# Kernel optimization log

Hardware: AMD Instinct MI355X
Metric: run time of the kernel (lower is better)

Reference implementation:

```python
import jax, jax.numpy as jnp
import numpy as np

N = 100000   # nodes
E = 1600000  # edges
NF = 128     # nfeat
NH = 64      # nhid
NC = 16      # nclass
C = 1.0      # curvature
EPS = 1e-15
PROJ_EPS = 4e-3  # float32 boundary eps used by HGCN PoincareBall
SQC = C ** 0.5


def _norm(v):
    return jnp.maximum(jnp.linalg.norm(v, axis=-1, keepdims=True), EPS)


def _artanh(v):
    return jnp.arctanh(jnp.clip(v, -1.0 + 1e-7, 1.0 - 1e-7))


def proj(p):
    # clip to the open ball of radius (1-eps)/sqrt(c)
    n = _norm(p)
    maxnorm = (1.0 - PROJ_EPS) / SQC
    return jnp.where(n > maxnorm, p / n * maxnorm, p)


def expmap0(u):
    n = _norm(u)
    return jnp.tanh(SQC * n) * u / (SQC * n)


def logmap0(p):
    n = _norm(p)
    return _artanh(SQC * n) * p / (SQC * n)


def mobius_add(x, y):
    x2 = jnp.sum(x * x, axis=-1, keepdims=True)
    y2 = jnp.sum(y * y, axis=-1, keepdims=True)
    xy = jnp.sum(x * y, axis=-1, keepdims=True)
    num = (1.0 + 2.0 * C * xy + C * y2) * x + (1.0 - C * x2) * y
    den = 1.0 + 2.0 * C * xy + (C ** 2) * x2 * y2
    return num / jnp.maximum(den, EPS)


def mobius_matvec(W, p):
    # W: [out, in], p: [N, in] on the ball
    pn = _norm(p)
    mp = p @ W.T  # [N, out]
    mpn = jnp.linalg.norm(mp, axis=-1, keepdims=True)
    res = jnp.tanh(mpn / pn * _artanh(SQC * pn)) * mp / (SQC * jnp.maximum(mpn, EPS))
    return jnp.where(mpn <= EPS, jnp.zeros_like(res), res)


def setup_inputs() -> dict:
    key = jax.random.key(0)
    ks = jax.random.split(key, 16)
    inp = {
        "x": jax.random.normal(ks[0], (N, NF), dtype=jnp.float32),
        "src": jax.random.randint(ks[1], (E,), 0, N, dtype=jnp.int32),
        "dst": jax.random.randint(ks[2], (E,), 0, N, dtype=jnp.int32),
        "adj_val": jax.random.uniform(ks[3], (E,), dtype=jnp.float32) * 0.0625,
        "W1": jax.random.normal(ks[4], (NH, NF), dtype=jnp.float32) / np.sqrt(NF),
        "b1": jnp.zeros((NH,), dtype=jnp.float32),
        "W2": jax.random.normal(ks[5], (NH, NH), dtype=jnp.float32) / np.sqrt(NH),
        "b2": jnp.zeros((NH,), dtype=jnp.float32),
        "W3": jax.random.normal(ks[6], (NH, NH), dtype=jnp.float32) / np.sqrt(NH),
        "b3": jnp.zeros((NH,), dtype=jnp.float32),
        "W4": jax.random.normal(ks[7], (NH // 2, NH), dtype=jnp.float32) / np.sqrt(NH),
        "b4": jnp.zeros((NH // 2,), dtype=jnp.float32),
        "W5": jax.random.normal(ks[8], (NC, NH // 2), dtype=jnp.float32) / np.sqrt(NH // 2),
        "b5": jnp.zeros((NC,), dtype=jnp.float32),
    }
    return inp


def _hgc_layer(h, W, b, src, dst, adj_val):
    # HypLinear: mobius matvec + hyperbolic bias
    res = proj(mobius_matvec(W, h))
    hyp_b = proj(expmap0(b[None, :]))
    res = proj(mobius_add(res, hyp_b))
    # HypAgg: aggregate in tangent space at origin via sparse adj
    ht = logmap0(res)                                   # [N, d]
    msg = adj_val[:, None] * ht[src]                    # [E, d]
    agg = jax.ops.segment_sum(msg, dst, num_segments=N)  # [N, d]
    res = proj(expmap0(agg))
    # HypAct: relu in tangent space, re-map to ball
    res = proj(expmap0(jax.nn.relu(logmap0(res))))
    return res


def reference(x, src, dst, adj_val, W1, b1, W2, b2, W3, b3, W4, b4, W5, b5):
    h = proj(expmap0(x))  # map Euclidean features to the ball (proj_tan0 = identity)
    h = _hgc_layer(h, W1, b1, src, dst, adj_val)
    h = _hgc_layer(h, W2, b2, src, dst, adj_val)
    h = _hgc_layer(h, W3, b3, src, dst, adj_val)
    t = logmap0(h)  # back to tangent space for the Euclidean head
    z = jax.nn.relu(t @ W4.T + b4)
    return jax.nn.log_softmax(z @ W5.T + b5, axis=-1)  # [N, nclass]
```

## Files before the change

### kernel.cpp

```cpp
#include <hip/hip_runtime.h>
#include <hip/hip_bf16.h>
#include <hip/hip_fp16.h>
#include <math.h>

#define NFEAT 128
#define NHID  64
#define ATH996 3.106303f
#define CHUNK 4096

typedef __attribute__((ext_vector_type(8))) short short8;
typedef __attribute__((ext_vector_type(4))) float floatx4;
typedef unsigned short ushort_t;
typedef unsigned long long u64;

__device__ __forceinline__ float wave_sum(float v) {
#pragma unroll
    for (int m = 1; m < 64; m <<= 1) v += __shfl_xor(v, m, 64);
    return v;
}

__device__ __forceinline__ float fast_tanh(float x) {
    float e = __expf(2.f * x);
    return 1.f - 2.f / (e + 1.f);
}

__device__ __forceinline__ float artanh_clip(float v) {
    const float lim = 0.99999988f;
    v = fminf(fmaxf(v, -lim), lim);
    return 0.5f * __logf((1.f + v) / (1.f - v));
}

__device__ __forceinline__ unsigned pack2(float a, float b) {
    __hip_bfloat16 x = __float2bfloat16(a), y = __float2bfloat16(b);
    ushort_t ux = *(ushort_t*)&x, uy = *(ushort_t*)&y;
    return (unsigned)ux | ((unsigned)uy << 16);
}

__device__ __forceinline__ ushort_t f2bf(float f) {
    __hip_bfloat16 h = __float2bfloat16(f);
    return *(ushort_t*)&h;
}

__device__ __forceinline__ float pe_adj(unsigned p) {
    return __half2float(__ushort_as_half((ushort_t)(p & 0x7fffu)));
}


__global__ __launch_bounds__(256) void k_bhist(const int* __restrict__ dst,
        int* __restrict__ gBktCnt, int e, int nb) {
    __shared__ int cnt[512];
    int tid = threadIdx.x;
    for (int t = tid; t < nb; t += 256) cnt[t] = 0;
    __syncthreads();
    int start = blockIdx.x * CHUNK, end = min(e, start + CHUNK);
    for (int i = start + tid; i < end; i += 256)
        atomicAdd(&cnt[dst[i] >> 8], 1);
    __syncthreads();
    for (int t = tid; t < nb; t += 256)
        if (cnt[t]) atomicAdd(&gBktCnt[t], cnt[t]);
}

__global__ __launch_bounds__(256) void k_bscan(const int* __restrict__ gBktCnt,
        int* __restrict__ gBktBase, int* __restrict__ gCur,
        int* __restrict__ off, int nb, int n, int e) {
    __shared__ int s[256];
    int tid = threadIdx.x;
    int base = tid * 4;
    int c0 = (base + 0 < nb) ? gBktCnt[base + 0] : 0;
    int c1 = (base + 1 < nb) ? gBktCnt[base + 1] : 0;
    int c2 = (base + 2 < nb) ? gBktCnt[base + 2] : 0;
    int c3 = (base + 3 < nb) ? gBktCnt[base + 3] : 0;
    int tsum = c0 + c1 + c2 + c3;
    s[tid] = tsum; __syncthreads();
    for (int o = 1; o < 256; o <<= 1) {
        int v = (tid >= o) ? s[tid - o] : 0;
        __syncthreads();
        s[tid] += v;
        __syncthreads();
    }
    int ex = s[tid] - tsum;
    int e0 = ex, e1 = ex + c0, e2 = ex + c0 + c1, e3 = ex + c0 + c1 + c2;
    if (base + 0 < nb) { gBktBase[base + 0] = e0; gCur[base + 0] = e0; }
    if (base + 1 < nb) { gBktBase[base + 1] = e1; gCur[base + 1] = e1; }
    if (base + 2 < nb) { gBktBase[base + 2] = e2; gCur[base + 2] = e2; }
    if (base + 3 < nb) { gBktBase[base + 3] = e3; gCur[base + 3] = e3; }
    if (tid == 255) gBktBase[nb] = s[255];
    if (tid == 0) off[n] = e;
}

__global__ __launch_bounds__(256) void k_bscatter(const int* __restrict__ dst,
        const int* __restrict__ src, const float* __restrict__ adj,
        int* __restrict__ gCur, u64* __restrict__ gStage, int e, int nb) {
    __shared__ u64 stage[CHUNK];
    __shared__ int cnt[512], excl[512], rcnt[512], myBase[512], s[256];
    int tid = threadIdx.x;
    int start = blockIdx.x * CHUNK, end = min(e, start + CHUNK);
    for (int t = tid; t < nb; t += 256) { cnt[t] = 0; rcnt[t] = 0; }
    __syncthreads();
    for (int i = start + tid; i < end; i += 256)
        atomicAdd(&cnt[dst[i] >> 8], 1);
    __syncthreads();
    int v0 = (2 * tid < nb) ? cnt[2 * tid] : 0;
    int v1 = (2 * tid + 1 < nb) ? cnt[2 * tid + 1] : 0;
    int tsum = v0 + v1;
    s[tid] = tsum; __syncthreads();
    for (int o = 1; o < 256; o <<= 1) {
        int v = (tid >= o) ? s[tid - o] : 0;
        __syncthreads();
        s[tid] += v;
        __syncthreads();
    }
    int ex = s[tid] - tsum;
    if (2 * tid < nb) excl[2 * tid] = ex;
    if (2 * tid + 1 < nb) excl[2 * tid + 1] = ex + v0;
    __syncthreads();
    for (int t = tid; t < nb; t += 256)
        if (cnt[t]) myBase[t] = atomicAdd(&gCur[t], cnt[t]);
    for (int i = start + tid; i < end; i += 256) {
        int d = dst[i];
        int b = d >> 8;
        unsigned ab = (unsigned)__half_as_ushort(__float2half(adj[i])) & 0x7fffu;
        u64 u = ((u64)(unsigned)d << 32) |
                (u64)(((unsigned)src[i] << 15) | ab);
        int r = atomicAdd(&rcnt[b], 1);
        stage[excl[b] + r] = u;
    }
    __syncthreads();
    int sz = end - start;
    for (int j = tid; j < sz; j += 256) {
        u64 u = stage[j];
        int b = (int)(u >> 40) & 0x1ff;
        gStage[myBase[b] + (j - excl[b])] = u;
    }
}

__global__ __launch_bounds__(256) void k_bfinal(const u64* __restrict__ gStage,
        const int* __restrict__ gBktBase, int* __restrict__ off,
        unsigned* __restrict__ pe, int n) {
    __shared__ int ncnt[256], nexcl[256], rcnt[256], s[256];
    int tid = threadIdx.x, b = blockIdx.x;
    int ebeg = gBktBase[b], eend = gBktBase[b + 1];
    int nbeg = b << 8;
    ncnt[tid] = 0; rcnt[tid] = 0;
    __syncthreads();
    for (int j = ebeg + tid; j < eend; j += 256) {
        int dl = ((int)(gStage[j] >> 32) & 0x1ffff) - nbeg;
        atomicAdd(&ncnt[dl], 1);
    }
    __syncthreads();
    int v = ncnt[tid];
    s[tid] = v; __syncthreads();
    for (int o = 1; o < 256; o <<= 1) {
        int t2 = (tid >= o) ? s[tid - o] : 0;
        __syncthreads();
        s[tid] += t2;
        __syncthreads();
    }
    nexcl[tid] = s[tid] - v;
    if (nbeg + tid < n) off[nbeg + tid] = ebeg + nexcl[tid];
    __syncthreads();
    for (int j = ebeg + tid; j < eend; j += 256) {
        u64 u = gStage[j];
        int dl = ((int)(u >> 32) & 0x1ffff) - nbeg;
        int r = atomicAdd(&rcnt[dl], 1);
        pe[ebeg + nexcl[dl] + r] = (unsigned)u;
    }
}

__global__ __launch_bounds__(256) void k_prep(
        const float* __restrict__ W1, const float* __restrict__ W2,
        const float* __restrict__ W3, const float* __restrict__ W4,
        const float* __restrict__ W5, const float* __restrict__ b1,
        const float* __restrict__ b2, const float* __restrict__ b3,
        ushort_t* __restrict__ Bpk1, ushort_t* __restrict__ Bpk2,
        ushort_t* __restrict__ Bpk3, ushort_t* __restrict__ Bpk4,
        ushort_t* __restrict__ Bpk5, float* __restrict__ hbs,
        float* __restrict__ hbns, int* __restrict__ gBktCnt, int nb) {
    int bid = blockIdx.x, tid = threadIdx.x;
    if (bid >= 75) {
        for (int t = tid; t < nb; t += 256) gBktCnt[t] = 0;
        return;
    }
    if (bid < 64) {
        const float* W; ushort_t* Bpk; int K, o;
        if (bid < 32)      { W = W1; Bpk = Bpk1; K = 128; o = bid * 256 + tid; }
        else if (bid < 48) { W = W2; Bpk = Bpk2; K = 64;  o = (bid - 32) * 256 + tid; }
        else               { W = W3; Bpk = Bpk3; K = 64;  o = (bid - 48) * 256 + tid; }
        int j = o & 7, c = (o >> 3) & 15, nf = (o >> 7) & 3, hi = (o >> 9) & 3,
            ks = o >> 11;
        Bpk[o] = f2bf(W[(nf * 16 + c) * K + ks * 32 + hi * 8 + j]);
    } else if (bid < 72) {
        int o = (bid - 64) * 256 + tid;
        int j = o & 7, c = (o >> 3) & 15, nf = (o >> 7) & 1, hi = (o >> 8) & 3,
            ks = o >> 10;
        Bpk4[o] = f2bf(W4[(nf * 16 + c) * 64 + ks * 32 + hi * 8 + j]);
    } else if (bid < 74) {
        int o = (bid - 72) * 256 + tid;
        if (o < 512) {
            int j = o & 7, c = (o >> 3) & 15, hi = o >> 7;
            Bpk5[o] = f2bf(W5[c * 32 + hi * 8 + j]);
        }
    } else {
        if (tid < 192) {
            int wv = tid >> 6, lane = tid & 63;
            const float* b = (wv == 0) ? b1 : (wv == 1) ? b2 : b3;
            float bv = b[lane];
            float bn = fmaxf(sqrtf(wave_sum(bv * bv)), 1e-15f);
            float th = fast_tanh(bn);
            float f = th / bn;
            float hn = th;
            if (th > 0.996f) { f = 0.996f / bn; hn = 0.996f; }
            hbs[wv * 64 + lane] = bv * f;
            if (lane == 0) hbns[wv] = hn;
        }
    }
}

__device__ __forceinline__ void epi_row(const floatx4* acc, int r, float pn,
        float hbn, const float* __restrict__ hb, int c, float outv[4]) {
    float pp = 0.f;
#pragma unroll
    for (int nf = 0; nf < 4; ++nf) pp += acc[nf][r] * acc[nf][r];
#pragma unroll
    for (int m = 1; m < 16; m <<= 1) pp += __shfl_xor(pp, m, 64);
    float mpn = sqrtf(pp);
    float an = artanh_clip(pn);
    if (hbn <= 1e-15f) {
        float targ = (mpn / pn) * an;
        float scale = (targ > ATH996) ? (ATH996 / mpn) : (an / pn);
        if (mpn <= 1e-15f) scale = 0.f;
#pragma unroll
        for (int nf = 0; nf < 4; ++nf) outv[nf] = acc[nf][r] * scale;
    } else {
        float targ = (mpn / pn) * an;
        float th = fast_tanh(targ);
        float rn = fminf(th, 0.996f);
        float rs = (mpn <= 1e-15f) ? 0.f : (rn / mpn);
        float res[4], xyp = 0.f;
#pragma unroll
        for (int nf = 0; nf < 4; ++nf) {
            res[nf] = acc[nf][r] * rs;
            xyp += res[nf] * hb[nf * 16 + c];
        }
#pragma unroll
        for (int m = 1; m < 16; m <<= 1) xyp += __shfl_xor(xyp, m, 64);
        float x2 = rn * rn, y2 = hbn * hbn;
        float den = fmaxf(1.f + 2.f * xyp + x2 * y2, 1e-15f);
        float ca = (1.f + 2.f * xyp + y2) / den, cb = (1.f - x2) / den;
        float mv[4], mm = 0.f;
#pragma unroll
        for (int nf = 0; nf < 4; ++nf) {
            mv[nf] = ca * res[nf] + cb * hb[nf * 16 + c];
            mm += mv[nf] * mv[nf];
        }
#pragma unroll
        for (int m = 1; m < 16; m <<= 1) mm += __shfl_xor(mm, m, 64);
        float mn = sqrtf(mm);
        float mc = fminf(fmaxf(mn, 1e-15f), 0.996f);
        float msc = ((mn > 0.996f) ? (0.996f / mn) : 1.f) * artanh_clip(mc) / mc;
#pragma unroll
        for (int nf = 0; nf < 4; ++nf) outv[nf] = mv[nf] * msc;
    }
}

__global__ __launch_bounds__(256) void k_gemm1(
        const float* __restrict__ x, const ushort_t* __restrict__ Bpk,
        const float* __restrict__ hb, const float* __restrict__ hbn_p,
        ushort_t* __restrict__ htout, int n) {
    constexpr int RB = 256;
    __shared__ __align__(16) unsigned char As[64 * RB];
    __shared__ float pns[64];
    int tid = threadIdx.x, wv = tid >> 6, lane = tid & 63;
    int rowBase = blockIdx.x * 64;
#pragma unroll
    for (int it = 0; it < 16; ++it) {
        int row = wv * 16 + it, rg = rowBase + row;
        float2 v = make_float2(0.f, 0.f);
        if (rg < n) v = *(const float2*)(x + (size_t)rg * NFEAT + lane * 2);
        float ss = wave_sum(v.x * v.x + v.y * v.y);
        float nr = fmaxf(sqrtf(ss), 1e-15f);
        float th = fast_tanh(nr);
        float f = th / nr;
        float pn = fmaxf(th, 1e-15f);
        if (th > 0.996f) { f = 0.996f / nr; pn = 0.996f; }
        unsigned byte = (unsigned)(row * RB + lane * 4) ^ ((row & 7) << 4);
        *(unsigned*)(As + byte) = pack2(v.x * f, v.y * f);
        if (lane == 0) pns[row] = pn;
    }
    int hi = lane >> 4, c = lane & 15;
    short8 bf[4][4];
#pragma unroll
    for (int ks = 0; ks < 4; ++ks)
#pragma unroll
        for (int nf = 0; nf < 4; ++nf)
            bf[ks][nf] = *(const short8*)(Bpk + (((size_t)(ks * 4 + hi) * 4 + nf) * 16 + c) * 8);
    floatx4 acc[4];
#pragma unroll
    for (int nf = 0; nf < 4; ++nf)
#pragma unroll
        for (int r = 0; r < 4; ++r) acc[nf][r] = 0.f;
    int arow = wv * 16 + c;
#pragma unroll
    for (int ks = 0; ks < 4; ++ks) {
        unsigned byte = (unsigned)(arow * RB + ks * 64 + hi * 16) ^ ((arow & 7) << 4);
        short8 af = *(const short8*)(As + byte);
#pragma unroll
        for (int nf = 0; nf < 4; ++nf)
            acc[nf] = __builtin_amdgcn_mfma_f32_16x16x32_bf16(af, bf[ks][nf], acc[nf], 0, 0, 0);
    }
    float hbn = hbn_p[0];
#pragma unroll
    for (int r = 0; r < 4; ++r) {
        int row = wv * 16 + hi * 4 + r, rg = rowBase + row;
        float outv[4];
        epi_row(acc, r, pns[row], hbn, hb, c, outv);
        if (rg < n) {
#pragma unroll
            for (int nf = 0; nf < 4; ++nf)
                htout[(size_t)rg * 64 + nf * 16 + c] = f2bf(outv[nf]);
        }
    }
}

__global__ __launch_bounds__(256) void k_gemm64(
        const ushort_t* __restrict__ h, const float* __restrict__ nrm_in,
        const ushort_t* __restrict__ Bpk, const float* __restrict__ hb,
        const float* __restrict__ hbn_p, ushort_t* __restrict__ htout, int n) {
    constexpr int RB = 128;
    __shared__ __align__(16) unsigned char As[64 * RB];
    int tid = threadIdx.x, wv = tid >> 6, lane = tid & 63;
    int rowBase = blockIdx.x * 64;
#pragma unroll
    for (int it = 0; it < 8; ++it) {
        int row = wv * 16 + it * 2 + (lane >> 5), rg = rowBase + row;
        int cl = lane & 31;
        unsigned pk = 0;
        if (rg < n) pk = *(const unsigned*)(h + (size_t)rg * 64 + cl * 2);
        unsigned byte = (unsigned)(row * RB + cl * 4) ^ ((row & 7) << 4);
        *(unsigned*)(As + byte) = pk;
    }
    int hi = lane >> 4, c = lane & 15;
    short8 bf[2][4];
#pragma unroll
    for (int ks = 0; ks < 2; ++ks)
#pragma unroll
        for (int nf = 0; nf < 4; ++nf)
            bf[ks][nf] = *(const short8*)(Bpk + (((size_t)(ks * 4 + hi) * 4 + nf) * 16 + c) * 8);
    floatx4 acc[4];
#pragma unroll
    for (int nf = 0; nf < 4; ++nf)
#pragma unroll
        for (int r = 0; r < 4; ++r) acc[nf][r] = 0.f;
    int arow = wv * 16 + c;
#pragma unroll
    for (int ks = 0; ks < 2; ++ks) {
        unsigned byte = (unsigned)(arow * RB + ks * 64 + hi * 16) ^ ((arow & 7) << 4);
        short8 af = *(const short8*)(As + byte);
#pragma unroll
        for (int nf = 0; nf < 4; ++nf)
            acc[nf] = __builtin_amdgcn_mfma_f32_16x16x32_bf16(af, bf[ks][nf], acc[nf], 0, 0, 0);
    }
    float hbn = hbn_p[0];
#pragma unroll
    for (int r = 0; r < 4; ++r) {
        int row = wv * 16 + hi * 4 + r, rg = rowBase + row;
        float pn = (rg < n) ? nrm_in[rg] : 1e-15f;
        float outv[4];
        epi_row(acc, r, pn, hbn, hb, c, outv);
        if (rg < n) {
#pragma unroll
            for (int nf = 0; nf < 4; ++nf)
                htout[(size_t)rg * 64 + nf * 16 + c] = f2bf(outv[nf]);
        }
    }
}

template <bool TANGENT_OUT>
__global__ __launch_bounds__(256) void k_agg_act(
        const ushort_t* __restrict__ ht, const int* __restrict__ off,
        const unsigned* __restrict__ pe, ushort_t* __restrict__ hout,
        float* __restrict__ nrm_out, int n) {
    int tid = threadIdx.x;
    int grp = tid >> 4, l = tid & 15;
    int node = blockIdx.x * 16 + grp;
    if (node >= n) return;
    int beg = off[node], end = off[node + 1];
    const char* hb8 = (const char*)ht + l * 8;
    float a0[4] = {0.f, 0.f, 0.f, 0.f};
    float a1[4] = {0.f, 0.f, 0.f, 0.f};
    float a2[4] = {0.f, 0.f, 0.f, 0.f};
    float a3[4] = {0.f, 0.f, 0.f, 0.f};
    int e = beg;
    for (; e + 3 < end; e += 4) {
        unsigned p0 = pe[e], p1 = pe[e + 1], p2 = pe[e + 2], p3 = pe[e + 3];
        uint2 r0 = *(const uint2*)(hb8 + ((size_t)(p0 >> 15) << 7));
        uint2 r1 = *(const uint2*)(hb8 + ((size_t)(p1 >> 15) << 7));
        uint2 r2 = *(const uint2*)(hb8 + ((size_t)(p2 >> 15) << 7));
        uint2 r3 = *(const uint2*)(hb8 + ((size_t)(p3 >> 15) << 7));
        float w0 = pe_adj(p0), w1 = pe_adj(p1), w2 = pe_adj(p2), w3 = pe_adj(p3);
        a0[0] = fmaf(w0, __uint_as_float(r0.x << 16), a0[0]);
        a0[1] = fmaf(w0, __uint_as_float(r0.x & 0xffff0000u), a0[1]);
        a0[2] = fmaf(w0, __uint_as_float(r0.y << 16), a0[2]);
        a0[3] = fmaf(w0, __uint_as_float(r0.y & 0xffff0000u), a0[3]);
        a1[0] = fmaf(w1, __uint_as_float(r1.x << 16), a1[0]);
        a1[1] = fmaf(w1, __uint_as_float(r1.x & 0xffff0000u), a1[1]);
        a1[2] = fmaf(w1, __uint_as_float(r1.y << 16), a1[2]);
        a1[3] = fmaf(w1, __uint_as_float(r1.y & 0xffff0000u), a1[3]);
        a2[0] = fmaf(w2, __uint_as_float(r2.x << 16), a2[0]);
        a2[1] = fmaf(w2, __uint_as_float(r2.x & 0xffff0000u), a2[1]);
        a2[2] = fmaf(w2, __uint_as_float(r2.y << 16), a2[2]);
        a2[3] = fmaf(w2, __uint_as_float(r2.y & 0xffff0000u), a2[3]);
        a3[0] = fmaf(w3, __uint_as_float(r3.x << 16), a3[0]);
        a3[1] = fmaf(w3, __uint_as_float(r3.x & 0xffff0000u), a3[1]);
        a3[2] = fmaf(w3, __uint_as_float(r3.y << 16), a3[2]);
        a3[3] = fmaf(w3, __uint_as_float(r3.y & 0xffff0000u), a3[3]);
    }
    for (; e < end; ++e) {
        unsigned p = pe[e];
        uint2 r = *(const uint2*)(hb8 + ((size_t)(p >> 15) << 7));
        float w = pe_adj(p);
        a0[0] = fmaf(w, __uint_as_float(r.x << 16), a0[0]);
        a0[1] = fmaf(w, __uint_as_float(r.x & 0xffff0000u), a0[1]);
        a0[2] = fmaf(w, __uint_as_float(r.y << 16), a0[2]);
        a0[3] = fmaf(w, __uint_as_float(r.y & 0xffff0000u), a0[3]);
    }
    float f0 = (a0[0] + a1[0]) + (a2[0] + a3[0]);
    float f1 = (a0[1] + a1[1]) + (a2[1] + a3[1]);
    float f2 = (a0[2] + a1[2]) + (a2[2] + a3[2]);
    float f3 = (a0[3] + a1[3]) + (a2[3] + a3[3]);
    float ss = f0 * f0 + f1 * f1 + f2 * f2 + f3 * f3;
#pragma unroll
    for (int m = 1; m < 16; m <<= 1) ss += __shfl_xor(ss, m, 64);
    float un = fmaxf(sqrtf(ss), 1e-15f);
    float thu = fast_tanh(un);
    float pf = thu / un, pn = thu;
    if (thu > 0.996f) { pf = 0.996f / un; pn = 0.996f; }
    float pnc = fmaxf(pn, 1e-15f);
    float ls = artanh_clip(pnc) / pnc * pf;
    float t0 = fmaxf(ls * f0, 0.f), t1 = fmaxf(ls * f1, 0.f);
    float t2 = fmaxf(ls * f2, 0.f), t3 = fmaxf(ls * f3, 0.f);
    float ss2 = t0 * t0 + t1 * t1 + t2 * t2 + t3 * t3;
#pragma unroll
    for (int m = 1; m < 16; m <<= 1) ss2 += __shfl_xor(ss2, m, 64);
    float tn = fmaxf(sqrtf(ss2), 1e-15f);
    uint2 ov;
    if (TANGENT_OUT) {
        float sc = (tn > ATH996) ? (ATH996 / tn) : 1.f;
        ov = make_uint2(pack2(t0 * sc, t1 * sc), pack2(t2 * sc, t3 * sc));
    } else {
        float tht = fast_tanh(tn);
        float rf = tht / tn, rn = tht;
        if (tht > 0.996f) { rf = 0.996f / tn; rn = 0.996f; }
        ov = make_uint2(pack2(rf * t0, rf * t1), pack2(rf * t2, rf * t3));
        if (l == 0) nrm_out[node] = fmaxf(rn, 1e-15f);
    }
    *(uint2*)((char*)hout + (size_t)node * 128 + l * 8) = ov;
}

__global__ __launch_bounds__(256) void k_head(
        const ushort_t* __restrict__ t_in, const ushort_t* __restrict__ Bpk4,
        const float* __restrict__ b4, const ushort_t* __restrict__ Bpk5,
        const float* __restrict__ b5, float* __restrict__ out, int n) {
    constexpr int RB = 128;
    __shared__ __align__(16) unsigned char As[64 * RB];
    __shared__ __align__(16) unsigned char Zs[4][16 * 80];
    int tid = threadIdx.x, wv = tid >> 6, lane = tid & 63;
    int rowBase = blockIdx.x * 64;
#pragma unroll
    for (int it = 0; it < 8; ++it) {
        int row = wv * 16 + it * 2 + (lane >> 5), rg = rowBase + row;
        int cl = lane & 31;
        unsigned pk = 0;
        if (rg < n) pk = *(const unsigned*)(t_in + (size_t)rg * 64 + cl * 2);
        unsigned byte = (unsigned)(row * RB + cl * 4) ^ ((row & 7) << 4);
        *(unsigned*)(As + byte) = pk;
    }
    int hi = lane >> 4, c = lane & 15;
    short8 bf4[2][2];
#pragma unroll
    for (int ks = 0; ks < 2; ++ks)
#pragma unroll
        for (int nf = 0; nf < 2; ++nf)
            bf4[ks][nf] = *(const short8*)(Bpk4 + (((size_t)(ks * 4 + hi) * 2 + nf) * 16 + c) * 8);
    floatx4 acc[2];
#pragma unroll
    for (int nf = 0; nf < 2; ++nf)
#pragma unroll
        for (int r = 0; r < 4; ++r) acc[nf][r] = 0.f;
    int arow = wv * 16 + c;
#pragma unroll
    for (int ks = 0; ks < 2; ++ks) {
        unsigned byte = (unsigned)(arow * RB + ks * 64 + hi * 16) ^ ((arow & 7) << 4);
        short8 af = *(const short8*)(As + byte);
#pragma unroll
        for (int nf = 0; nf < 2; ++nf)
            acc[nf] = __builtin_amdgcn_mfma_f32_16x16x32_bf16(af, bf4[ks][nf], acc[nf], 0, 0, 0);
    }
    float bb0 = b4[c], bb1 = b4[16 + c];
#pragma unroll
    for (int r = 0; r < 4; ++r) {
        int zr = hi * 4 + r;
        *(ushort_t*)(Zs[wv] + zr * 80 + c * 2) = f2bf(fmaxf(acc[0][r] + bb0, 0.f));
        *(ushort_t*)(Zs[wv] + zr * 80 + (16 + c) * 2) = f2bf(fmaxf(acc[1][r] + bb1, 0.f));
    }
    short8 bf5 = *(const short8*)(Bpk5 + ((size_t)(hi * 16 + c)) * 8);
    short8 zf = *(const short8*)(Zs[wv] + c * 80 + hi * 16);
    floatx4 acc5;
#pragma unroll
    for (int r = 0; r < 4; ++r) acc5[r] = 0.f;
    acc5 = __builtin_amdgcn_mfma_f32_16x16x32_bf16(zf, bf5, acc5, 0, 0, 0);
    float b5v = b5[c];
#pragma unroll
    for (int r = 0; r < 4; ++r) {
        float y = acc5[r] + b5v;
        float mx = y;
#pragma unroll
        for (int mk = 1; mk < 16; mk <<= 1) mx = fmaxf(mx, __shfl_xor(mx, mk, 64));
        float sm = __expf(y - mx);
#pragma unroll
        for (int mk = 1; mk < 16; mk <<= 1) sm += __shfl_xor(sm, mk, 64);
        int rg = rowBase + wv * 16 + hi * 4 + r;
        if (rg < n) out[(size_t)rg * 16 + c] = y - mx - __logf(sm);
    }
}

extern "C" void kernel_launch(void* const* d_in, const int* in_sizes, int n_in,
                              void* d_out, int out_size, void* d_ws, size_t ws_size,
                              hipStream_t stream) {
    const float* x   = (const float*)d_in[0];
    const int*   src = (const int*)d_in[1];
    const int*   dst = (const int*)d_in[2];
    const float* adj = (const float*)d_in[3];
    const float* W1  = (const float*)d_in[4];  const float* b1 = (const float*)d_in[5];
    const float* W2  = (const float*)d_in[6];  const float* b2 = (const float*)d_in[7];
    const float* W3  = (const float*)d_in[8];  const float* b3 = (const float*)d_in[9];
    const float* W4  = (const float*)d_in[10]; const float* b4 = (const float*)d_in[11];
    const float* W5  = (const float*)d_in[12]; const float* b5 = (const float*)d_in[13];
    float* out = (float*)d_out;

    const int N = in_sizes[0] / NFEAT;
    const int E = in_sizes[1];
    const int NB = (N + 255) >> 8;

    char* w = (char*)d_ws;
    auto alloc = [&](size_t bytes) {
        char* p = w; w += (bytes + 255) & ~(size_t)255; return p;
    };
    int* off      = (int*)alloc((size_t)(N + 1) * 4);
    int* gBktCnt  = (int*)alloc((size_t)NB * 4);
    int* gBktBase = (int*)alloc((size_t)(NB + 1) * 4);
    int* gCur     = (int*)alloc((size_t)NB * 4);
    u64* gStage   = (u64*)alloc((size_t)E * 8);
    unsigned* pe  = (unsigned*)alloc((size_t)E * 4);
    ushort_t* B   = (ushort_t*)alloc((size_t)N * 64 * 2);
    ushort_t* D   = (ushort_t*)alloc((size_t)N * 64 * 2);
    float* nrm    = (float*)alloc((size_t)N * 4);
    float* hbs    = (float*)alloc(192 * 4);
    float* hbns   = (float*)alloc(4 * 4);
    ushort_t* Bpk1 = (ushort_t*)alloc(8192 * 2);
    ushort_t* Bpk2 = (ushort_t*)alloc(4096 * 2);
    ushort_t* Bpk3 = (ushort_t*)alloc(4096 * 2);
    ushort_t* Bpk4 = (ushort_t*)alloc(2048 * 2);
    ushort_t* Bpk5 = (ushort_t*)alloc(512 * 2);

    dim3 blk(256);
    int aggBlocks  = (N + 15) / 16;
    int gemmBlocks = (N + 63) / 64;
    int sortBlocks = (E + CHUNK - 1) / CHUNK;

    k_prep<<<76, blk, 0, stream>>>(W1, W2, W3, W4, W5, b1, b2, b3,
                                   Bpk1, Bpk2, Bpk3, Bpk4, Bpk5, hbs, hbns,
                                   gBktCnt, NB);

    k_gemm1<<<gemmBlocks, blk, 0, stream>>>(x, Bpk1, hbs, hbns, B, N);

    k_bhist<<<sortBlocks, blk, 0, stream>>>(dst, gBktCnt, E, NB);
    k_bscan<<<1, blk, 0, stream>>>(gBktCnt, gBktBase, gCur, off, NB, N, E);
    k_bscatter<<<sortBlocks, blk, 0, stream>>>(dst, src, adj, gCur, gStage, E, NB);
    k_bfinal<<<NB, blk, 0, stream>>>(gStage, gBktBase, off, pe, N);

    k_agg_act<false><<<aggBlocks, blk, 0, stream>>>(B, off, pe, D, nrm, N);
    k_gemm64<<<gemmBlocks, blk, 0, stream>>>(D, nrm, Bpk2, hbs + 64, hbns + 1, B, N);
    k_agg_act<false><<<aggBlocks, blk, 0, stream>>>(B, off, pe, D, nrm, N);
    k_gemm64<<<gemmBlocks, blk, 0, stream>>>(D, nrm, Bpk3, hbs + 128, hbns + 2, B, N);
    k_agg_act<true><<<aggBlocks, blk, 0, stream>>>(B, off, pe, D, nullptr, N);

    k_head<<<gemmBlocks, blk, 0, stream>>>(D, Bpk4, b4, Bpk5, b5, out, N);
}
```

Baseline: 236.9 us.

## Fuse edge histogram into first GEMM launch and widen row loads

Merges the destination-bucket histogram kernel into the first GEMM kernel as extra blocks, removing one launch and letting the two independent jobs overlap on the device. The first GEMM now loads raw x rows with wide float4 loads across 16-lane groups, stages them unscaled in bf16, and applies the expmap scale factor after the MFMA instead of before. The 64-wide GEMM and head kernels also switch to 8-byte row loads. Applying the scale after the matmul changes bf16 rounding slightly, and the merged kernel's shared memory grows with the histogram buffer.

```diff
diff --git a/kernel.cpp b/kernel.cpp
--- a/kernel.cpp
+++ b/kernel.cpp
@@ -45,20 +45,6 @@
     return __half2float(__ushort_as_half((ushort_t)(p & 0x7fffu)));
 }
 
-
-__global__ __launch_bounds__(256) void k_bhist(const int* __restrict__ dst,
-        int* __restrict__ gBktCnt, int e, int nb) {
-    __shared__ int cnt[512];
-    int tid = threadIdx.x;
-    for (int t = tid; t < nb; t += 256) cnt[t] = 0;
-    __syncthreads();
-    int start = blockIdx.x * CHUNK, end = min(e, start + CHUNK);
-    for (int i = start + tid; i < end; i += 256)
-        atomicAdd(&cnt[dst[i] >> 8], 1);
-    __syncthreads();
-    for (int t = tid; t < nb; t += 256)
-        if (cnt[t]) atomicAdd(&gBktCnt[t], cnt[t]);
-}
 
 __global__ __launch_bounds__(256) void k_bscan(const int* __restrict__ gBktCnt,
         int* __restrict__ gBktBase, int* __restrict__ gCur,
@@ -216,11 +202,11 @@
     }
 }
 
-__device__ __forceinline__ void epi_row(const floatx4* acc, int r, float pn,
+__device__ __forceinline__ void epi_vals(const float vin[4], float pn,
         float hbn, const float* __restrict__ hb, int c, float outv[4]) {
     float pp = 0.f;
 #pragma unroll
-    for (int nf = 0; nf < 4; ++nf) pp += acc[nf][r] * acc[nf][r];
+    for (int nf = 0; nf < 4; ++nf) pp += vin[nf] * vin[nf];
 #pragma unroll
     for (int m = 1; m < 16; m <<= 1) pp += __shfl_xor(pp, m, 64);
     float mpn = sqrtf(pp);
@@ -230,7 +216,7 @@
         float scale = (targ > ATH996) ? (ATH996 / mpn) : (an / pn);
         if (mpn <= 1e-15f) scale = 0.f;
 #pragma unroll
-        for (int nf = 0; nf < 4; ++nf) outv[nf] = acc[nf][r] * scale;
+        for (int nf = 0; nf < 4; ++nf) outv[nf] = vin[nf] * scale;
     } else {
         float targ = (mpn / pn) * an;
         float th = fast_tanh(targ);
@@ -239,7 +225,7 @@
         float res[4], xyp = 0.f;
 #pragma unroll
         for (int nf = 0; nf < 4; ++nf) {
-            res[nf] = acc[nf][r] * rs;
+            res[nf] = vin[nf] * rs;
             xyp += res[nf] * hb[nf * 16 + c];
         }
 #pragma unroll
@@ -263,29 +249,55 @@
     }
 }
 
-__global__ __launch_bounds__(256) void k_gemm1(
+__global__ __launch_bounds__(256) void k_gemm1_hist(
         const float* __restrict__ x, const ushort_t* __restrict__ Bpk,
         const float* __restrict__ hb, const float* __restrict__ hbn_p,
-        ushort_t* __restrict__ htout, int n) {
+        ushort_t* __restrict__ htout, int n, int gBlocks,
+        const int* __restrict__ dst, int* __restrict__ gBktCnt, int e, int nb) {
     constexpr int RB = 256;
     __shared__ __align__(16) unsigned char As[64 * RB];
-    __shared__ float pns[64];
-    int tid = threadIdx.x, wv = tid >> 6, lane = tid & 63;
+    __shared__ float pns[64], fs[64];
+    __shared__ int cnt[512];
+    int tid = threadIdx.x;
+    if ((int)blockIdx.x >= gBlocks) {
+        for (int t = tid; t < nb; t += 256) cnt[t] = 0;
+        __syncthreads();
+        int start = ((int)blockIdx.x - gBlocks) * CHUNK, end = min(e, start + CHUNK);
+        for (int i = start + tid; i < end; i += 256)
+            atomicAdd(&cnt[dst[i] >> 8], 1);
+        __syncthreads();
+        for (int t = tid; t < nb; t += 256)
+            if (cnt[t]) atomicAdd(&gBktCnt[t], cnt[t]);
+        return;
+    }
+    int wv = tid >> 6, lane = tid & 63;
+    int grp = lane >> 4, l = lane & 15;
     int rowBase = blockIdx.x * 64;
 #pragma unroll
-    for (int it = 0; it < 16; ++it) {
-        int row = wv * 16 + it, rg = rowBase + row;
-        float2 v = make_float2(0.f, 0.f);
-        if (rg < n) v = *(const float2*)(x + (size_t)rg * NFEAT + lane * 2);
-        float ss = wave_sum(v.x * v.x + v.y * v.y);
-        float nr = fmaxf(sqrtf(ss), 1e-15f);
-        float th = fast_tanh(nr);
-        float f = th / nr;
-        float pn = fmaxf(th, 1e-15f);
-        if (th > 0.996f) { f = 0.996f / nr; pn = 0.996f; }
-        unsigned byte = (unsigned)(row * RB + lane * 4) ^ ((row & 7) << 4);
-        *(unsigned*)(As + byte) = pack2(v.x * f, v.y * f);
-        if (lane == 0) pns[row] = pn;
+    for (int it = 0; it < 4; ++it) {
+        int row = wv * 16 + it * 4 + grp, rg = rowBase + row;
+        float4 va = make_float4(0.f, 0.f, 0.f, 0.f), vb = va;
+        if (rg < n) {
+            const float4* xr = (const float4*)(x + (size_t)rg * NFEAT + l * 8);
+            va = xr[0]; vb = xr[1];
+        }
+        uint4 pk;
+        pk.x = pack2(va.x, va.y); pk.y = pack2(va.z, va.w);
+        pk.z = pack2(vb.x, vb.y); pk.w = pack2(vb.z, vb.w);
+        unsigned byte = (unsigned)(row * RB + l * 16) ^ ((row & 7) << 4);
+        *(uint4*)(As + byte) = pk;
+        float ss = va.x * va.x + va.y * va.y + va.z * va.z + va.w * va.w +
+                   vb.x * vb.x + vb.y * vb.y + vb.z * vb.z + vb.w * vb.w;
+#pragma unroll
+        for (int m = 1; m < 16; m <<= 1) ss += __shfl_xor(ss, m, 64);
+        if (l == 0) {
+            float nr = fmaxf(sqrtf(ss), 1e-15f);
+            float th = fast_tanh(nr);
+            float f = th / nr;
+            float pn = fmaxf(th, 1e-15f);
+            if (th > 0.996f) { f = 0.996f / nr; pn = 0.996f; }
+            pns[row] = pn; fs[row] = f;
+        }
     }
     int hi = lane >> 4, c = lane & 15;
     short8 bf[4][4];
@@ -312,8 +324,11 @@
 #pragma unroll
     for (int r = 0; r < 4; ++r) {
         int row = wv * 16 + hi * 4 + r, rg = rowBase + row;
-        float outv[4];
-        epi_row(acc, r, pns[row], hbn, hb, c, outv);
+        float f = fs[row];
+        float vin[4], outv[4];
+#pragma unroll
+        for (int nf = 0; nf < 4; ++nf) vin[nf] = acc[nf][r] * f;
+        epi_vals(vin, pns[row], hbn, hb, c, outv);
         if (rg < n) {
 #pragma unroll
             for (int nf = 0; nf < 4; ++nf)
@@ -329,15 +344,15 @@
     constexpr int RB = 128;
     __shared__ __align__(16) unsigned char As[64 * RB];
     int tid = threadIdx.x, wv = tid >> 6, lane = tid & 63;
+    int grp = lane >> 4, l = lane & 15;
     int rowBase = blockIdx.x * 64;
 #pragma unroll
-    for (int it = 0; it < 8; ++it) {
-        int row = wv * 16 + it * 2 + (lane >> 5), rg = rowBase + row;
-        int cl = lane & 31;
-        unsigned pk = 0;
-        if (rg < n) pk = *(const unsigned*)(h + (size_t)rg * 64 + cl * 2);
-        unsigned byte = (unsigned)(row * RB + cl * 4) ^ ((row & 7) << 4);
-        *(unsigned*)(As + byte) = pk;
+    for (int it = 0; it < 4; ++it) {
+        int row = wv * 16 + it * 4 + grp, rg = rowBase + row;
+        uint2 pk = make_uint2(0u, 0u);
+        if (rg < n) pk = *(const uint2*)(h + (size_t)rg * 64 + l * 4);
+        unsigned byte = (unsigned)(row * RB + l * 8) ^ ((row & 7) << 4);
+        *(uint2*)(As + byte) = pk;
     }
     int hi = lane >> 4, c = lane & 15;
     short8 bf[2][4];
@@ -365,8 +380,10 @@
     for (int r = 0; r < 4; ++r) {
         int row = wv * 16 + hi * 4 + r, rg = rowBase + row;
         float pn = (rg < n) ? nrm_in[rg] : 1e-15f;
-        float outv[4];
-        epi_row(acc, r, pn, hbn, hb, c, outv);
+        float vin[4], outv[4];
+#pragma unroll
+        for (int nf = 0; nf < 4; ++nf) vin[nf] = acc[nf][r];
+        epi_vals(vin, pn, hbn, hb, c, outv);
         if (rg < n) {
 #pragma unroll
             for (int nf = 0; nf < 4; ++nf)
@@ -465,15 +482,15 @@
     __shared__ __align__(16) unsigned char As[64 * RB];
     __shared__ __align__(16) unsigned char Zs[4][16 * 80];
     int tid = threadIdx.x, wv = tid >> 6, lane = tid & 63;
+    int grp = lane >> 4, l = lane & 15;
     int rowBase = blockIdx.x * 64;
 #pragma unroll
-    for (int it = 0; it < 8; ++it) {
-        int row = wv * 16 + it * 2 + (lane >> 5), rg = rowBase + row;
-        int cl = lane & 31;
-        unsigned pk = 0;
-        if (rg < n) pk = *(const unsigned*)(t_in + (size_t)rg * 64 + cl * 2);
-        unsigned byte = (unsigned)(row * RB + cl * 4) ^ ((row & 7) << 4);
-        *(unsigned*)(As + byte) = pk;
+    for (int it = 0; it < 4; ++it) {
+        int row = wv * 16 + it * 4 + grp, rg = rowBase + row;
+        uint2 pk = make_uint2(0u, 0u);
+        if (rg < n) pk = *(const uint2*)(t_in + (size_t)rg * 64 + l * 4);
+        unsigned byte = (unsigned)(row * RB + l * 8) ^ ((row & 7) << 4);
+        *(uint2*)(As + byte) = pk;
     }
     int hi = lane >> 4, c = lane & 15;
     short8 bf4[2][2];
@@ -572,9 +589,9 @@
                                    Bpk1, Bpk2, Bpk3, Bpk4, Bpk5, hbs, hbns,
                                    gBktCnt, NB);
 
-    k_gemm1<<<gemmBlocks, blk, 0, stream>>>(x, Bpk1, hbs, hbns, B, N);
-
-    k_bhist<<<sortBlocks, blk, 0, stream>>>(dst, gBktCnt, E, NB);
+    k_gemm1_hist<<<gemmBlocks + sortBlocks, blk, 0, stream>>>(
+        x, Bpk1, hbs, hbns, B, N, gemmBlocks, dst, gBktCnt, E, NB);
+
     k_bscan<<<1, blk, 0, stream>>>(gBktCnt, gBktBase, gCur, off, NB, N, E);
     k_bscatter<<<sortBlocks, blk, 0, stream>>>(dst, src, adj, gCur, gStage, E, NB);
     k_bfinal<<<NB, blk, 0, stream>>>(gStage, gBktBase, off, pe, N);
```

New measurement: 218.7 us. 7.7% less time.
